# Performance work log

Hardware: AMD Instinct MI355X
Metric: run time of the kernel (lower is better)

## Reference

```python
import jax, jax.numpy as jnp
import numpy as np

N = 16384
E = 524288
IN_DIM = 512
HID = 256
NCLS = 64


def setup_inputs() -> dict:
    key = jax.random.key(0)
    k1, k2, k3, k4, k5, k6 = jax.random.split(key, 6)
    X = jax.random.normal(k1, (N, IN_DIM), dtype=jnp.float32)
    edge_index = jax.random.randint(k2, (2, E), 0, N, dtype=jnp.int64)
    # torch nn.Linear params: y = x @ W.T + b
    W1 = jax.random.normal(k3, (HID, IN_DIM), dtype=jnp.float32) * (1.0 / np.sqrt(IN_DIM))
    b1 = jax.random.normal(k4, (HID,), dtype=jnp.float32) * 0.01
    W2 = jax.random.normal(k5, (NCLS, HID), dtype=jnp.float32) * (1.0 / np.sqrt(HID))
    b2 = jax.random.normal(k6, (NCLS,), dtype=jnp.float32) * 0.01
    return {"X": X, "edge_index": edge_index, "W1": W1, "b1": b1, "W2": W2, "b2": b2}


def _build_a_hat(edge_index, n):
    # Dense adjacency via scatter-set, exactly as the torch code does.
    A = jnp.zeros((n, n), dtype=jnp.float32)
    A = A.at[edge_index[0], edge_index[1]].set(1.0)
    A = A + A.T
    A = (A > 0).astype(jnp.float32)
    A = A + jnp.eye(n, dtype=jnp.float32)
    # symmetric normalization: D^-1/2 A D^-1/2 (diag matmuls == broadcast)
    deg = A.sum(axis=1)
    dis = jnp.power(deg + 1e-8, -0.5)
    return dis[:, None] * A * dis[None, :]


def reference(X, edge_index, W1, b1, W2, b2):
    n = X.shape[0]
    A_hat = _build_a_hat(edge_index, n)
    H = A_hat @ X                      # [N, in_dim]
    H = H @ W1.T + b1                  # lin1
    H = jax.nn.relu(H)
    # dropout is identity in eval mode
    H = A_hat @ H                      # [N, hidden]
    H = H @ W2.T + b2                  # lin2 -> [N, num_classes]
    return H
```

## Files before the change

kernel.cpp:

```cpp
#include <hip/hip_runtime.h>
#include <stdint.h>

#define N_NODES 16384
#define N_EDGES 524288
#define IN_DIM  512
#define HID     256
#define NCLS    64
#define LSTRIDE 192
#define NBKT    1024
#define SCAP    24
#define NBBLK   256
#define GEMM_BLKS 256

typedef __bf16 bf16x8 __attribute__((ext_vector_type(8)));
typedef float  f32x4  __attribute__((ext_vector_type(4)));
typedef unsigned int u32x4 __attribute__((ext_vector_type(4)));

__device__ __forceinline__ unsigned short f2bf(float f) {
    unsigned int u = __float_as_uint(f);
    u += 0x7FFFu + ((u >> 16) & 1u);
    return (unsigned short)(u >> 16);
}
__device__ __forceinline__ float bflo(unsigned int u) { return __uint_as_float(u << 16); }
__device__ __forceinline__ float bfhi(unsigned int u) { return __uint_as_float(u & 0xFFFF0000u); }

__device__ __forceinline__ void bucket_body(
    int blk, const void* __restrict__ ep, unsigned int* __restrict__ cnt,
    unsigned int* __restrict__ gbuf, char* smem) {
    unsigned int* lcnt = (unsigned int*)smem;
    __shared__ int sflag;
    const int tid = threadIdx.x;
    if (tid == 0) {
        const int* p = (const int*)ep;
        int odd = 1;
        for (int k = 0; k < 64; ++k)
            if (p[2 * k + 1] != 0) odd = 0;
        sflag = odd;
    }
    for (int b = tid; b < NBKT; b += 256) lcnt[b] = 0;
    __syncthreads();

    const int e0 = blk * 2048 + tid;
    int s[8], d[8];
    if (sflag) {
        const long long* p = (const long long*)ep;
        #pragma unroll
        for (int q = 0; q < 8; ++q) {
            s[q] = (int)p[e0 + q * 256];
            d[q] = (int)p[N_EDGES + e0 + q * 256];
        }
    } else {
        const int* p = (const int*)ep;
        #pragma unroll
        for (int q = 0; q < 8; ++q) {
            s[q] = p[e0 + q * 256];
            d[q] = p[N_EDGES + e0 + q * 256];
        }
    }
    unsigned int* myslice = gbuf + (size_t)blk * NBKT * SCAP;
    #pragma unroll
    for (int q = 0; q < 8; ++q) {
        int b0 = s[q] >> 4, b1 = d[q] >> 4;
        unsigned int sl0 = atomicAdd(&lcnt[b0], 1u);
        unsigned int sl1 = atomicAdd(&lcnt[b1], 1u);
        if (sl0 < SCAP)
            myslice[b0 * SCAP + sl0] =
                ((unsigned int)(s[q] & 15) << 14) | (unsigned int)d[q];
        if (sl1 < SCAP)
            myslice[b1 * SCAP + sl1] =
                ((unsigned int)(d[q] & 15) << 14) | (unsigned int)s[q];
    }
    __syncthreads();
    for (int b = tid; b < NBKT; b += 256)
        cnt[(size_t)b * NBBLK + blk] = min(lcnt[b], (unsigned int)SCAP);
}

__global__ __launch_bounds__(256) void build_csr(
    const unsigned int* __restrict__ cnt, const unsigned int* __restrict__ gbuf,
    float* __restrict__ dis, int* __restrict__ ncnt,
    unsigned short* __restrict__ lists) {
    __shared__ unsigned int bml[16 * 512];
    const int tid = threadIdx.x;
    const int bkt = blockIdx.x;
    const int node0 = bkt * 16;
    #pragma unroll
    for (int q = 0; q < 32; ++q) bml[tid + q * 256] = 0;
    __syncthreads();
    {
        const unsigned int c = cnt[(size_t)bkt * NBBLK + tid];
        const unsigned int* sp = gbuf + ((size_t)tid * NBKT + bkt) * SCAP;
        for (unsigned int l = 0; l < c; ++l) {
            unsigned int e = sp[l];
            unsigned int local = e >> 14, nbr = e & 16383u;
            atomicOr(&bml[local * 512 + (nbr >> 5)], 1u << (nbr & 31u));
        }
    }
    __syncthreads();
    const int wid = tid >> 6, lane = tid & 63;
    for (int nn = wid; nn < 16; nn += 4) {
        const int node = node0 + nn;
        const unsigned int* row = bml + nn * 512 + lane * 8;
        unsigned int w[8];
        int c = 0;
        #pragma unroll
        for (int j = 0; j < 8; ++j) { w[j] = row[j]; c += __popc(w[j]); }
        int inc = c;
        #pragma unroll
        for (int dd = 1; dd < 64; dd <<= 1) {
            int t = __shfl_up(inc, dd);
            if (lane >= dd) inc += t;
        }
        int total = __shfl(inc, 63);
        unsigned short* dst = lists + (size_t)node * LSTRIDE + (inc - c);
        int k = 0;
        #pragma unroll
        for (int j = 0; j < 8; ++j) {
            unsigned int bits = w[j];
            int base = (lane * 8 + j) * 32;
            while (bits) {
                int b = __ffs(bits) - 1;
                bits &= bits - 1;
                dst[k++] = (unsigned short)(base + b);
            }
        }
        if (lane == 63) {
            lists[(size_t)node * LSTRIDE + total] = (unsigned short)node;
            ncnt[node] = total + 1;
            dis[node] = 1.0f / sqrtf((float)(total + 1) + 1e-8f);
        }
    }
}

template <bool F32>
__device__ __forceinline__ uint4 ld_chunk(const void* __restrict__ G,
                                          size_t row, int KD, int k0, int s) {
    if constexpr (F32) {
        const float* g = (const float*)G + row * KD + k0 + s * 8;
        float4 v0 = *(const float4*)g;
        float4 v1 = *(const float4*)(g + 4);
        uint4 w;
        w.x = (unsigned int)f2bf(v0.x) | ((unsigned int)f2bf(v0.y) << 16);
        w.y = (unsigned int)f2bf(v0.z) | ((unsigned int)f2bf(v0.w) << 16);
        w.z = (unsigned int)f2bf(v1.x) | ((unsigned int)f2bf(v1.y) << 16);
        w.w = (unsigned int)f2bf(v1.z) | ((unsigned int)f2bf(v1.w) << 16);
        return w;
    } else {
        return *(const uint4*)((const unsigned short*)G + row * KD + k0 + s * 8);
    }
}

template <int BM, int BN, int KD, int ND, bool AF32, bool BF32>
__device__ __forceinline__ void gemm_body(
    int bx, int by, const void* __restrict__ Ag, const void* __restrict__ Bg,
    unsigned short* __restrict__ Cg, const float* __restrict__ dis, char* smem) {
    constexpr int FM = BM / 32, FN = BN / 32;
    constexpr int NK = KD / 64;
    unsigned short* Asm = (unsigned short*)smem;
    unsigned short* Bsm = (unsigned short*)smem + BM * 64;
    const int tid = threadIdx.x;
    const int lane = tid & 63;
    const int wid = tid >> 6;
    const int wm = wid >> 1, wn = wid & 1;
    const int m0 = bx * BM, n0 = by * BN;

    uint4 ra[BM / 32], rb[BN / 32];
    #pragma unroll
    for (int q = 0; q < BM / 32; ++q) {
        int cch = tid + 256 * q, r = cch >> 3, s = cch & 7;
        ra[q] = ld_chunk<AF32>(Ag, (size_t)(m0 + r), KD, 0, s);
    }
    #pragma unroll
    for (int q = 0; q < BN / 32; ++q) {
        int cch = tid + 256 * q, r = cch >> 3, s = cch & 7;
        rb[q] = ld_chunk<BF32>(Bg, (size_t)(n0 + r), KD, 0, s);
    }

    f32x4 acc[FM][FN] = {};

    for (int kt = 0; kt < NK; ++kt) {
        __syncthreads();
        #pragma unroll
        for (int q = 0; q < BM / 32; ++q) {
            int cch = tid + 256 * q, r = cch >> 3, s = cch & 7;
            *(uint4*)((char*)Asm + r * 128 + ((s ^ (r & 7)) << 4)) = ra[q];
        }
        #pragma unroll
        for (int q = 0; q < BN / 32; ++q) {
            int cch = tid + 256 * q, r = cch >> 3, s = cch & 7;
            *(uint4*)((char*)Bsm + r * 128 + ((s ^ (r & 7)) << 4)) = rb[q];
        }
        __syncthreads();
        if (kt + 1 < NK) {
            int k0 = (kt + 1) * 64;
            #pragma unroll
            for (int q = 0; q < BM / 32; ++q) {
                int cch = tid + 256 * q, r = cch >> 3, s = cch & 7;
                ra[q] = ld_chunk<AF32>(Ag, (size_t)(m0 + r), KD, k0, s);
            }
            #pragma unroll
            for (int q = 0; q < BN / 32; ++q) {
                int cch = tid + 256 * q, r = cch >> 3, s = cch & 7;
                rb[q] = ld_chunk<BF32>(Bg, (size_t)(n0 + r), KD, k0, s);
            }
        }
        #pragma unroll
        for (int ks = 0; ks < 2; ++ks) {
            bf16x8 af[FM], bg[FN];
            #pragma unroll
            for (int i = 0; i < FM; ++i) {
                int row = wm * (BM / 2) + i * 16 + (lane & 15);
                int slot = (ks * 4 + (lane >> 4)) ^ (row & 7);
                af[i] = *(const bf16x8*)((const char*)Asm + row * 128 + slot * 16);
            }
            #pragma unroll
            for (int j = 0; j < FN; ++j) {
                int row = wn * (BN / 2) + j * 16 + (lane & 15);
                int slot = (ks * 4 + (lane >> 4)) ^ (row & 7);
                bg[j] = *(const bf16x8*)((const char*)Bsm + row * 128 + slot * 16);
            }
            #pragma unroll
            for (int i = 0; i < FM; ++i)
                #pragma unroll
                for (int j = 0; j < FN; ++j)
                    acc[i][j] = __builtin_amdgcn_mfma_f32_16x16x32_bf16(af[i], bg[j], acc[i][j], 0, 0, 0);
        }
    }

    #pragma unroll
    for (int i = 0; i < FM; ++i) {
        #pragma unroll
        for (int e = 0; e < 4; ++e) {
            int row = m0 + wm * (BM / 2) + i * 16 + ((lane >> 4) << 2) + e;
            float dm = dis ? dis[row] : 1.0f;
            #pragma unroll
            for (int j = 0; j < FN; ++j) {
                int col = n0 + wn * (BN / 2) + j * 16 + (lane & 15);
                Cg[(size_t)row * ND + col] = f2bf(acc[i][j][e] * dm);
            }
        }
    }
}

__global__ __launch_bounds__(256) void bucket_gemm(
    const float* __restrict__ X, const float* __restrict__ W1,
    unsigned short* __restrict__ Y, const void* __restrict__ ep,
    unsigned int* __restrict__ cnt, unsigned int* __restrict__ gbuf) {
    __shared__ __align__(16) char smem[(128 + 128) * 64 * 2];
    if (blockIdx.x < GEMM_BLKS) {
        int gb = blockIdx.x;
        gemm_body<128, 128, IN_DIM, HID, true, true>(
            gb & 127, gb >> 7, X, W1, Y, nullptr, smem);
    } else {
        bucket_body(blockIdx.x - GEMM_BLKS, ep, cnt, gbuf, smem);
    }
}

__global__ __launch_bounds__(256) void gemm2_k(
    const unsigned short* __restrict__ H1, const float* __restrict__ W2,
    unsigned short* __restrict__ Z, const float* __restrict__ dis) {
    __shared__ __align__(16) char smem[(128 + 64) * 64 * 2];
    gemm_body<128, 64, HID, NCLS, false, true>(blockIdx.x, 0, H1, W2, Z, dis, smem);
}

__global__ __launch_bounds__(256) void spmm_hid(
    const int* __restrict__ ncnt, const unsigned short* __restrict__ lists,
    const float* __restrict__ dis, const unsigned short* __restrict__ Yp,
    const float* __restrict__ bias, unsigned short* __restrict__ H1) {
    const int bid = blockIdx.x;
    const int r = bid & 7;
    const int fh = r >> 2;
    const int wid = threadIdx.x >> 6, lane = threadIdx.x & 63;
    const int i = (bid >> 3) * 16 + (r & 3) * 4 + wid;

    __shared__ uint2 sld[4][LSTRIDE];
    const int n = min(ncnt[i], LSTRIDE);
    for (int l = lane; l < n; l += 64) {
        int j = lists[(size_t)i * LSTRIDE + l];
        uint2 m;
        m.x = __float_as_uint(dis[j]);
        m.y = (unsigned int)j << 9;
        sld[wid][l] = m;
    }
    __syncthreads();

    const int qw = lane >> 4, p = lane & 15;
    const char* Ybase = (const char*)Yp + fh * 256 + p * 16;
    float acc[8] = {}, acc2[8] = {};
    int l = 0;
    for (; l + 8 <= n; l += 8) {
        uint2 m0 = sld[wid][l + qw];
        uint2 m1 = sld[wid][l + 4 + qw];
        uint4 u0 = *(const uint4*)(Ybase + m0.y);
        uint4 u1 = *(const uint4*)(Ybase + m1.y);
        float w0 = __uint_as_float(m0.x), w1 = __uint_as_float(m1.x);
        acc[0] = fmaf(w0, bflo(u0.x), acc[0]); acc[1] = fmaf(w0, bfhi(u0.x), acc[1]);
        acc[2] = fmaf(w0, bflo(u0.y), acc[2]); acc[3] = fmaf(w0, bfhi(u0.y), acc[3]);
        acc[4] = fmaf(w0, bflo(u0.z), acc[4]); acc[5] = fmaf(w0, bfhi(u0.z), acc[5]);
        acc[6] = fmaf(w0, bflo(u0.w), acc[6]); acc[7] = fmaf(w0, bfhi(u0.w), acc[7]);
        acc2[0] = fmaf(w1, bflo(u1.x), acc2[0]); acc2[1] = fmaf(w1, bfhi(u1.x), acc2[1]);
        acc2[2] = fmaf(w1, bflo(u1.y), acc2[2]); acc2[3] = fmaf(w1, bfhi(u1.y), acc2[3]);
        acc2[4] = fmaf(w1, bflo(u1.z), acc2[4]); acc2[5] = fmaf(w1, bfhi(u1.z), acc2[5]);
        acc2[6] = fmaf(w1, bflo(u1.w), acc2[6]); acc2[7] = fmaf(w1, bfhi(u1.w), acc2[7]);
    }
    for (; l < n; l += 4) {
        if (l + qw < n) {
            uint2 m = sld[wid][l + qw];
            uint4 u = *(const uint4*)(Ybase + m.y);
            float w = __uint_as_float(m.x);
            acc[0] = fmaf(w, bflo(u.x), acc[0]); acc[1] = fmaf(w, bfhi(u.x), acc[1]);
            acc[2] = fmaf(w, bflo(u.y), acc[2]); acc[3] = fmaf(w, bfhi(u.y), acc[3]);
            acc[4] = fmaf(w, bflo(u.z), acc[4]); acc[5] = fmaf(w, bfhi(u.z), acc[5]);
            acc[6] = fmaf(w, bflo(u.w), acc[6]); acc[7] = fmaf(w, bfhi(u.w), acc[7]);
        }
    }
    #pragma unroll
    for (int k = 0; k < 8; ++k) {
        acc[k] += acc2[k];
        acc[k] += __shfl_xor(acc[k], 16);
        acc[k] += __shfl_xor(acc[k], 32);
    }
    if (qw == 0) {
        float di = dis[i];
        float4 b0 = *(const float4*)&bias[fh * 128 + p * 8];
        float4 b1 = *(const float4*)&bias[fh * 128 + p * 8 + 4];
        float v0 = fmaxf(fmaf(di, acc[0], b0.x), 0.0f);
        float v1 = fmaxf(fmaf(di, acc[1], b0.y), 0.0f);
        float v2 = fmaxf(fmaf(di, acc[2], b0.z), 0.0f);
        float v3 = fmaxf(fmaf(di, acc[3], b0.w), 0.0f);
        float v4 = fmaxf(fmaf(di, acc[4], b1.x), 0.0f);
        float v5 = fmaxf(fmaf(di, acc[5], b1.y), 0.0f);
        float v6 = fmaxf(fmaf(di, acc[6], b1.z), 0.0f);
        float v7 = fmaxf(fmaf(di, acc[7], b1.w), 0.0f);
        u32x4 o;
        o.x = (unsigned int)f2bf(v0) | ((unsigned int)f2bf(v1) << 16);
        o.y = (unsigned int)f2bf(v2) | ((unsigned int)f2bf(v3) << 16);
        o.z = (unsigned int)f2bf(v4) | ((unsigned int)f2bf(v5) << 16);
        o.w = (unsigned int)f2bf(v6) | ((unsigned int)f2bf(v7) << 16);
        __builtin_nontemporal_store(o, (u32x4*)&H1[(size_t)i * 256 + fh * 128 + p * 8]);
    }
}

__global__ __launch_bounds__(256) void spmm_out(
    const int* __restrict__ ncnt, const unsigned short* __restrict__ lists,
    const float* __restrict__ dis, const unsigned short* __restrict__ Zp,
    const float* __restrict__ bias, float* __restrict__ out) {
    const int wid = threadIdx.x >> 6, lane = threadIdx.x & 63;
    const int i = blockIdx.x * 4 + wid;
    __shared__ unsigned int sl[4][LSTRIDE];
    const int n = min(ncnt[i], LSTRIDE);
    for (int l = lane; l < n; l += 64)
        sl[wid][l] = (unsigned int)lists[(size_t)i * LSTRIDE + l] << 7;
    __syncthreads();

    const int g = lane >> 3, p = lane & 7;
    const char* Zbase = (const char*)Zp + p * 16;
    float acc[8] = {}, acc2[8] = {};
    int l = 0;
    for (; l + 16 <= n; l += 16) {
        uint4 u0 = *(const uint4*)(Zbase + sl[wid][l + g]);
        uint4 u1 = *(const uint4*)(Zbase + sl[wid][l + 8 + g]);
        acc[0] += bflo(u0.x); acc[1] += bfhi(u0.x);
        acc[2] += bflo(u0.y); acc[3] += bfhi(u0.y);
        acc[4] += bflo(u0.z); acc[5] += bfhi(u0.z);
        acc[6] += bflo(u0.w); acc[7] += bfhi(u0.w);
        acc2[0] += bflo(u1.x); acc2[1] += bfhi(u1.x);
        acc2[2] += bflo(u1.y); acc2[3] += bfhi(u1.y);
        acc2[4] += bflo(u1.z); acc2[5] += bfhi(u1.z);
        acc2[6] += bflo(u1.w); acc2[7] += bfhi(u1.w);
    }
    for (; l < n; l += 8) {
        if (l + g < n) {
            uint4 u = *(const uint4*)(Zbase + sl[wid][l + g]);
            acc[0] += bflo(u.x); acc[1] += bfhi(u.x);
            acc[2] += bflo(u.y); acc[3] += bfhi(u.y);
            acc[4] += bflo(u.z); acc[5] += bfhi(u.z);
            acc[6] += bflo(u.w); acc[7] += bfhi(u.w);
        }
    }
    #pragma unroll
    for (int k = 0; k < 8; ++k) {
        acc[k] += acc2[k];
        acc[k] += __shfl_xor(acc[k], 8);
        acc[k] += __shfl_xor(acc[k], 16);
        acc[k] += __shfl_xor(acc[k], 32);
    }
    if (lane < 8) {
        float di = dis[i];
        float4 b0 = *(const float4*)&bias[p * 8];
        float4 b1 = *(const float4*)&bias[p * 8 + 4];
        f32x4 o0, o1;
        o0.x = fmaf(di, acc[0], b0.x); o0.y = fmaf(di, acc[1], b0.y);
        o0.z = fmaf(di, acc[2], b0.z); o0.w = fmaf(di, acc[3], b0.w);
        o1.x = fmaf(di, acc[4], b1.x); o1.y = fmaf(di, acc[5], b1.y);
        o1.z = fmaf(di, acc[6], b1.z); o1.w = fmaf(di, acc[7], b1.w);
        float* op = &out[(size_t)i * 64 + p * 8];
        __builtin_nontemporal_store(o0, (f32x4*)op);
        __builtin_nontemporal_store(o1, (f32x4*)(op + 4));
    }
}

extern "C" void kernel_launch(void* const* d_in, const int* in_sizes, int n_in,
                              void* d_out, int out_size, void* d_ws, size_t ws_size,
                              hipStream_t stream) {
    const float* X  = (const float*)d_in[0];
    const void*  EI = d_in[1];
    const float* W1 = (const float*)d_in[2];
    const float* b1 = (const float*)d_in[3];
    const float* W2 = (const float*)d_in[4];
    const float* b2 = (const float*)d_in[5];
    float* out = (float*)d_out;

    char* ws = (char*)d_ws;
    char* p = ws;
    unsigned int* cnt  = (unsigned int*)p;       p += (size_t)NBBLK * NBKT * 4;
    unsigned int* gbuf = (unsigned int*)p;       p += (size_t)NBBLK * NBKT * SCAP * 4;
    float* dis = (float*)p;                      p += (size_t)N_NODES * 4;
    int* ncnt = (int*)p;                         p += (size_t)N_NODES * 4;
    unsigned short* lists = (unsigned short*)p;  p += (size_t)N_NODES * LSTRIDE * 2;
    unsigned short* Y   = (unsigned short*)p;    p += (size_t)N_NODES * HID * 2;
    unsigned short* H1  = (unsigned short*)p;    p += (size_t)N_NODES * HID * 2;
    unsigned short* Z   = (unsigned short*)p;    p += (size_t)N_NODES * NCLS * 2;

    bucket_gemm<<<GEMM_BLKS + NBBLK, 256, 0, stream>>>(X, W1, Y, EI, cnt, gbuf);
    build_csr<<<NBKT, 256, 0, stream>>>(cnt, gbuf, dis, ncnt, lists);
    spmm_hid<<<2 * N_NODES / 4, 256, 0, stream>>>(ncnt, lists, dis, Y, b1, H1);
    gemm2_k<<<N_NODES / 128, 256, 0, stream>>>(H1, W2, Z, dis);
    spmm_out<<<N_NODES / 4, 256, 0, stream>>>(ncnt, lists, dis, Z, b2, out);
}
```

Measured before the change: 107.6 us.

## Split GEMM1 across bucket and CSR kernels to overlap with graph build

```diff
diff --git a/kernel.cpp b/kernel.cpp
--- a/kernel.cpp
+++ b/kernel.cpp
@@ -11,6 +11,7 @@
 #define SCAP    24
 #define NBBLK   256
 #define GEMM_BLKS 256
+#define G1A     128
 
 typedef __bf16 bf16x8 __attribute__((ext_vector_type(8)));
 typedef float  f32x4  __attribute__((ext_vector_type(4)));
@@ -75,16 +76,19 @@
         cnt[(size_t)b * NBBLK + blk] = min(lcnt[b], (unsigned int)SCAP);
 }
 
-__global__ __launch_bounds__(256) void build_csr(
-    const unsigned int* __restrict__ cnt, const unsigned int* __restrict__ gbuf,
-    float* __restrict__ dis, int* __restrict__ ncnt,
-    unsigned short* __restrict__ lists) {
-    __shared__ unsigned int bml[16 * 512];
+__device__ __forceinline__ void csr_body(
+    int bkt, const unsigned int* __restrict__ cnt,
+    const unsigned int* __restrict__ gbuf, float* __restrict__ dis,
+    int* __restrict__ ncnt, unsigned short* __restrict__ lists, char* smem) {
+    unsigned int* bml = (unsigned int*)smem;
     const int tid = threadIdx.x;
-    const int bkt = blockIdx.x;
     const int node0 = bkt * 16;
-    #pragma unroll
-    for (int q = 0; q < 32; ++q) bml[tid + q * 256] = 0;
+    {
+        const u32x4 z = {0, 0, 0, 0};
+        #pragma unroll
+        for (int q = 0; q < 8; ++q)
+            ((u32x4*)bml)[tid + q * 256] = z;
+    }
     __syncthreads();
     {
         const unsigned int c = cnt[(size_t)bkt * NBBLK + tid];
@@ -246,12 +250,27 @@
     unsigned short* __restrict__ Y, const void* __restrict__ ep,
     unsigned int* __restrict__ cnt, unsigned int* __restrict__ gbuf) {
     __shared__ __align__(16) char smem[(128 + 128) * 64 * 2];
-    if (blockIdx.x < GEMM_BLKS) {
+    if (blockIdx.x < G1A) {
         int gb = blockIdx.x;
         gemm_body<128, 128, IN_DIM, HID, true, true>(
             gb & 127, gb >> 7, X, W1, Y, nullptr, smem);
     } else {
-        bucket_body(blockIdx.x - GEMM_BLKS, ep, cnt, gbuf, smem);
+        bucket_body(blockIdx.x - G1A, ep, cnt, gbuf, smem);
+    }
+}
+
+__global__ __launch_bounds__(256) void csr_gemm(
+    const float* __restrict__ X, const float* __restrict__ W1,
+    unsigned short* __restrict__ Y, const unsigned int* __restrict__ cnt,
+    const unsigned int* __restrict__ gbuf, float* __restrict__ dis,
+    int* __restrict__ ncnt, unsigned short* __restrict__ lists) {
+    __shared__ __align__(16) char smem[(128 + 128) * 64 * 2];
+    if (blockIdx.x < (GEMM_BLKS - G1A)) {
+        int gb = blockIdx.x + G1A;
+        gemm_body<128, 128, IN_DIM, HID, true, true>(
+            gb & 127, gb >> 7, X, W1, Y, nullptr, smem);
+    } else {
+        csr_body(blockIdx.x - (GEMM_BLKS - G1A), cnt, gbuf, dis, ncnt, lists, smem);
     }
 }
 
@@ -421,8 +440,9 @@
     unsigned short* H1  = (unsigned short*)p;    p += (size_t)N_NODES * HID * 2;
     unsigned short* Z   = (unsigned short*)p;    p += (size_t)N_NODES * NCLS * 2;
 
-    bucket_gemm<<<GEMM_BLKS + NBBLK, 256, 0, stream>>>(X, W1, Y, EI, cnt, gbuf);
-    build_csr<<<NBKT, 256, 0, stream>>>(cnt, gbuf, dis, ncnt, lists);
+    bucket_gemm<<<G1A + NBBLK, 256, 0, stream>>>(X, W1, Y, EI, cnt, gbuf);
+    csr_gemm<<<(GEMM_BLKS - G1A) + NBKT, 256, 0, stream>>>(X, W1, Y, cnt, gbuf,
+                                                           dis, ncnt, lists);
     spmm_hid<<<2 * N_NODES / 4, 256, 0, stream>>>(ncnt, lists, dis, Y, b1, H1);
     gemm2_k<<<N_NODES / 128, 256, 0, stream>>>(H1, W2, Z, dis);
     spmm_out<<<N_NODES / 4, 256, 0, stream>>>(ncnt, lists, dis, Z, b2, out);
```

After: 114.6 us. 1.07x slower.

## Replace fixed-capacity bucket slots with per-block counting-sorted edge buffers

Applied to the files above, without the earlier changes.

```diff
diff --git a/kernel.cpp b/kernel.cpp
--- a/kernel.cpp
+++ b/kernel.cpp
@@ -8,8 +8,9 @@
 #define NCLS    64
 #define LSTRIDE 192
 #define NBKT    1024
-#define SCAP    24
 #define NBBLK   256
+#define ENT     4096
+#define OFFSTRIDE 1032
 #define GEMM_BLKS 256
 
 typedef __bf16 bf16x8 __attribute__((ext_vector_type(8)));
@@ -25,24 +26,28 @@
 __device__ __forceinline__ float bfhi(unsigned int u) { return __uint_as_float(u & 0xFFFF0000u); }
 
 __device__ __forceinline__ void bucket_body(
-    int blk, const void* __restrict__ ep, unsigned int* __restrict__ cnt,
+    int blk, const void* __restrict__ ep, unsigned int* __restrict__ offbuf,
     unsigned int* __restrict__ gbuf, char* smem) {
-    unsigned int* lcnt = (unsigned int*)smem;
-    __shared__ int sflag;
+    unsigned int* lcnt   = (unsigned int*)smem;
+    unsigned int* loff   = lcnt + NBKT;
+    unsigned int* sorted = loff + NBKT;
+    unsigned int* wsum   = sorted + ENT;
+    int* sflag = (int*)(wsum + 4);
     const int tid = threadIdx.x;
     if (tid == 0) {
         const int* p = (const int*)ep;
         int odd = 1;
         for (int k = 0; k < 64; ++k)
             if (p[2 * k + 1] != 0) odd = 0;
-        sflag = odd;
-    }
-    for (int b = tid; b < NBKT; b += 256) lcnt[b] = 0;
+        *sflag = odd;
+    }
+    #pragma unroll
+    for (int q = 0; q < 4; ++q) lcnt[tid + q * 256] = 0;
     __syncthreads();
 
     const int e0 = blk * 2048 + tid;
     int s[8], d[8];
-    if (sflag) {
+    if (*sflag) {
         const long long* p = (const long long*)ep;
         #pragma unroll
         for (int q = 0; q < 8; ++q) {
@@ -57,39 +62,83 @@
             d[q] = p[N_EDGES + e0 + q * 256];
         }
     }
-    unsigned int* myslice = gbuf + (size_t)blk * NBKT * SCAP;
+    unsigned int meta[16];
     #pragma unroll
     for (int q = 0; q < 8; ++q) {
         int b0 = s[q] >> 4, b1 = d[q] >> 4;
         unsigned int sl0 = atomicAdd(&lcnt[b0], 1u);
         unsigned int sl1 = atomicAdd(&lcnt[b1], 1u);
-        if (sl0 < SCAP)
-            myslice[b0 * SCAP + sl0] =
-                ((unsigned int)(s[q] & 15) << 14) | (unsigned int)d[q];
-        if (sl1 < SCAP)
-            myslice[b1 * SCAP + sl1] =
-                ((unsigned int)(d[q] & 15) << 14) | (unsigned int)s[q];
-    }
-    __syncthreads();
-    for (int b = tid; b < NBKT; b += 256)
-        cnt[(size_t)b * NBBLK + blk] = min(lcnt[b], (unsigned int)SCAP);
+        meta[2 * q]     = (unsigned int)b0 | (sl0 << 10);
+        meta[2 * q + 1] = (unsigned int)b1 | (sl1 << 10);
+    }
+    __syncthreads();
+
+    const int lane = tid & 63, wv = tid >> 6;
+    unsigned int c0 = lcnt[4 * tid], c1 = lcnt[4 * tid + 1];
+    unsigned int c2 = lcnt[4 * tid + 2], c3 = lcnt[4 * tid + 3];
+    unsigned int p1 = c0 + c1, p2 = p1 + c2, tot = p2 + c3;
+    unsigned int inc = tot;
+    #pragma unroll
+    for (int dd = 1; dd < 64; dd <<= 1) {
+        unsigned int v = __shfl_up(inc, dd);
+        if (lane >= dd) inc += v;
+    }
+    if (lane == 63) wsum[wv] = inc;
+    __syncthreads();
+    unsigned int wbase = 0;
+    #pragma unroll
+    for (int w = 0; w < 3; ++w)
+        if (w < wv) wbase += wsum[w];
+    unsigned int base = wbase + inc - tot;
+    loff[4 * tid]     = base;
+    loff[4 * tid + 1] = base + c0;
+    loff[4 * tid + 2] = base + p1;
+    loff[4 * tid + 3] = base + p2;
+    {
+        uint4 ov;
+        ov.x = base; ov.y = base + c0; ov.z = base + p1; ov.w = base + p2;
+        *(uint4*)&offbuf[(size_t)blk * OFFSTRIDE + 4 * tid] = ov;
+        if (tid == 255) offbuf[(size_t)blk * OFFSTRIDE + 1024] = ENT;
+    }
+    __syncthreads();
+
+    #pragma unroll
+    for (int q = 0; q < 8; ++q) {
+        unsigned int m0 = meta[2 * q];
+        sorted[loff[m0 & 1023u] + (m0 >> 10)] =
+            ((unsigned int)(s[q] & 15) << 14) | (unsigned int)d[q];
+        unsigned int m1 = meta[2 * q + 1];
+        sorted[loff[m1 & 1023u] + (m1 >> 10)] =
+            ((unsigned int)(d[q] & 15) << 14) | (unsigned int)s[q];
+    }
+    __syncthreads();
+
+    #pragma unroll
+    for (int q = 0; q < 4; ++q)
+        ((uint4*)gbuf)[(size_t)blk * (ENT / 4) + tid + q * 256] =
+            ((const uint4*)sorted)[tid + q * 256];
 }
 
 __global__ __launch_bounds__(256) void build_csr(
-    const unsigned int* __restrict__ cnt, const unsigned int* __restrict__ gbuf,
+    const unsigned int* __restrict__ offbuf, const unsigned int* __restrict__ gbuf,
     float* __restrict__ dis, int* __restrict__ ncnt,
     unsigned short* __restrict__ lists) {
     __shared__ unsigned int bml[16 * 512];
     const int tid = threadIdx.x;
     const int bkt = blockIdx.x;
     const int node0 = bkt * 16;
-    #pragma unroll
-    for (int q = 0; q < 32; ++q) bml[tid + q * 256] = 0;
-    __syncthreads();
     {
-        const unsigned int c = cnt[(size_t)bkt * NBBLK + tid];
-        const unsigned int* sp = gbuf + ((size_t)tid * NBKT + bkt) * SCAP;
-        for (unsigned int l = 0; l < c; ++l) {
+        const u32x4 z = {0, 0, 0, 0};
+        #pragma unroll
+        for (int q = 0; q < 8; ++q)
+            ((u32x4*)bml)[tid + q * 256] = z;
+    }
+    __syncthreads();
+    {
+        const unsigned int st = offbuf[(size_t)tid * OFFSTRIDE + bkt];
+        const unsigned int en = offbuf[(size_t)tid * OFFSTRIDE + bkt + 1];
+        const unsigned int* sp = gbuf + (size_t)tid * ENT;
+        for (unsigned int l = st; l < en; ++l) {
             unsigned int e = sp[l];
             unsigned int local = e >> 14, nbr = e & 16383u;
             atomicOr(&bml[local * 512 + (nbr >> 5)], 1u << (nbr & 31u));
@@ -244,14 +293,14 @@
 __global__ __launch_bounds__(256) void bucket_gemm(
     const float* __restrict__ X, const float* __restrict__ W1,
     unsigned short* __restrict__ Y, const void* __restrict__ ep,
-    unsigned int* __restrict__ cnt, unsigned int* __restrict__ gbuf) {
+    unsigned int* __restrict__ offbuf, unsigned int* __restrict__ gbuf) {
     __shared__ __align__(16) char smem[(128 + 128) * 64 * 2];
     if (blockIdx.x < GEMM_BLKS) {
         int gb = blockIdx.x;
         gemm_body<128, 128, IN_DIM, HID, true, true>(
             gb & 127, gb >> 7, X, W1, Y, nullptr, smem);
     } else {
-        bucket_body(blockIdx.x - GEMM_BLKS, ep, cnt, gbuf, smem);
+        bucket_body(blockIdx.x - GEMM_BLKS, ep, offbuf, gbuf, smem);
     }
 }
 
@@ -412,8 +461,8 @@
 
     char* ws = (char*)d_ws;
     char* p = ws;
-    unsigned int* cnt  = (unsigned int*)p;       p += (size_t)NBBLK * NBKT * 4;
-    unsigned int* gbuf = (unsigned int*)p;       p += (size_t)NBBLK * NBKT * SCAP * 4;
+    unsigned int* offbuf = (unsigned int*)p;     p += (size_t)NBBLK * OFFSTRIDE * 4;
+    unsigned int* gbuf   = (unsigned int*)p;     p += (size_t)NBBLK * ENT * 4;
     float* dis = (float*)p;                      p += (size_t)N_NODES * 4;
     int* ncnt = (int*)p;                         p += (size_t)N_NODES * 4;
     unsigned short* lists = (unsigned short*)p;  p += (size_t)N_NODES * LSTRIDE * 2;
@@ -421,8 +470,8 @@
     unsigned short* H1  = (unsigned short*)p;    p += (size_t)N_NODES * HID * 2;
     unsigned short* Z   = (unsigned short*)p;    p += (size_t)N_NODES * NCLS * 2;
 
-    bucket_gemm<<<GEMM_BLKS + NBBLK, 256, 0, stream>>>(X, W1, Y, EI, cnt, gbuf);
-    build_csr<<<NBKT, 256, 0, stream>>>(cnt, gbuf, dis, ncnt, lists);
+    bucket_gemm<<<GEMM_BLKS + NBBLK, 256, 0, stream>>>(X, W1, Y, EI, offbuf, gbuf);
+    build_csr<<<NBKT, 256, 0, stream>>>(offbuf, gbuf, dis, ncnt, lists);
     spmm_hid<<<2 * N_NODES / 4, 256, 0, stream>>>(ncnt, lists, dis, Y, b1, H1);
     gemm2_k<<<N_NODES / 128, 256, 0, stream>>>(H1, W2, Z, dis);
     spmm_out<<<N_NODES / 4, 256, 0, stream>>>(ncnt, lists, dis, Z, b2, out);
```

After: 103.7 us. 1.04x faster.
